# Kernel optimization log

Hardware: AMD Instinct MI355X
Metric: run time of the kernel (lower is better)

Reference implementation:

```python
import jax, jax.numpy as jnp
import numpy as np

B, L, D, H, DH, DI, NL, V = 1, 2048, 1024, 16, 64, 4096, 12, 32000
EPS = 1e-5  # torch LayerNorm default eps
SCALE = 1.0 / DH ** 0.5


def _ln(x):
    # LayerNorm with elementwise_affine=False
    m = jnp.mean(x, axis=-1, keepdims=True)
    va = jnp.var(x, axis=-1, keepdims=True)
    return (x - m) / jnp.sqrt(va + EPS)


def setup_inputs() -> dict:
    key = jax.random.key(0)
    ks = jax.random.split(key, 12)
    s = 0.02
    return {
        "X": jax.random.randint(ks[0], (B, L), 0, V),
        "Y": jax.random.randint(ks[1], (B, L), 0, V),
        "emb": jax.random.normal(ks[2], (V, D), jnp.float32) * s,
        "u": jax.random.normal(ks[3], (H, DH), jnp.float32) * s,
        "v": jax.random.normal(ks[4], (H, DH), jnp.float32) * s,
        "Wqkv": jax.random.normal(ks[5], (NL, 3 * H * DH, D), jnp.float32) * s,
        "Wpe": jax.random.normal(ks[6], (NL, H * DH, D), jnp.float32) * s,
        "Wout": jax.random.normal(ks[7], (NL, D, H * DH), jnp.float32) * s,
        "W1": jax.random.normal(ks[8], (NL, DI, D), jnp.float32) * s,
        "b1": jnp.zeros((NL, DI), jnp.float32),
        "W2": jax.random.normal(ks[9], (NL, D, DI), jnp.float32) * s,
        "b2": jnp.zeros((NL, D), jnp.float32),
        "Wc": jax.random.normal(ks[10], (V, D), jnp.float32) * s,
        "bc": jnp.zeros((V,), jnp.float32),
    }


def _forward(X, emb, u, v, Wqkv, Wpe, Wout, W1, b1, W2, b2, Wc, bc):
    q_len = X.shape[1]
    k_len = q_len  # mems=None -> m_len=0
    h = emb[X]  # (B, L, D); d_embedding == d_model so no projection

    # sinusoidal relative position embedding over descending positions
    pos = jnp.arange(k_len - 1, -1, -1, dtype=h.dtype)
    inv_freq = 1.0 / (10000.0 ** (jnp.arange(0, D, 2, dtype=h.dtype) / D))
    pp = pos[:, None] * inv_freq[None, :]              # (k, D/2)
    pe = jnp.concatenate([jnp.sin(pp), jnp.cos(pp)], axis=1)[None]  # (1, k, D)

    # causal mask: triu(ones, diagonal=1 + m_len), m_len=0; True = masked
    mask = jnp.triu(jnp.ones((q_len, k_len), bool), k=1)

    def layer(hid, params):
        wqkv, wpe, wout, w1, bb1, w2, bb2 = params
        qkv = hid @ wqkv.T                              # (B, q, 3HD)
        Q, K, Vv = jnp.split(qkv, 3, axis=-1)
        Q = Q.reshape(B, q_len, H, DH)
        K = K.reshape(B, k_len, H, DH)
        Vv = Vv.reshape(B, k_len, H, DH)
        r = (pe @ wpe.T).reshape(B, k_len, H, DH)       # requires B == 1
        AC = jnp.einsum('bqhd,bkhd->bhqk', Q + u, K)
        # NOTE: original code calls relative_shift(BD) but DISCARDS the result,
        # so BD is used unshifted — we reproduce that faithfully.
        BD = jnp.einsum('bqhd,bkhd->bhqk', Q + v, r)
        score = (AC + BD) * SCALE
        score = jnp.where(mask[None, None], -jnp.inf, score)
        prob = jax.nn.softmax(score, axis=-1)
        av = jnp.einsum('bhqk,bkhd->bqhd', prob, Vv).reshape(B, q_len, H * DH)
        hid = _ln(hid + av @ wout.T)                    # post-norm attention
        ff = jax.nn.relu(hid @ w1.T + bb1) @ w2.T + bb2
        hid = _ln(hid + ff)                             # post-norm FFN
        return hid, None

    h, _ = jax.lax.scan(layer, h, (Wqkv, Wpe, Wout, W1, b1, W2, b2))
    logits = h @ Wc.T + bc                              # (B, L, V)
    return logits.reshape(B * q_len, V)


def reference(X, Y, emb, u, v, Wqkv, Wpe, Wout, W1, b1, W2, b2, Wc, bc):
    # Y only determines y_len; here y_len == q_len so the full hidden is used.
    return _forward(X, emb, u, v, Wqkv, Wpe, Wout, W1, b1, W2, b2, Wc, bc)
```

## Files before the change

### kernel.cpp

```cpp
#include <hip/hip_runtime.h>
#include <hip/hip_bf16.h>

#define L_ 2048
#define D_ 1024
#define H_ 16
#define DH_ 64
#define DI_ 4096
#define NL_ 12
#define V_ 32000
#define EPS_ 1e-5f
#define SCALE_ 0.125f
#define LOG2E_ 1.44269504f
#define KBLK 64

typedef __attribute__((ext_vector_type(8))) short short8;
typedef __attribute__((ext_vector_type(4))) float f32x4;
typedef __hip_bfloat16 bf16;

__device__ __forceinline__ void gload_lds16(const void* g, void* l) {
  __builtin_amdgcn_global_load_lds((const __attribute__((address_space(1))) void*)g,
                                   (__attribute__((address_space(3))) void*)l, 16, 0, 0);
}

template<int STORE_BF16, int BIAS, int RELU, int SPLITK>
__global__ __launch_bounds__(256)
void gemm_bt(const bf16* __restrict__ A, const bf16* __restrict__ B,
             void* __restrict__ C, const float* __restrict__ bias,
             int M, int N, int K, int lda, int ldb, int ldc,
             long long Astride, long long Bstride, long long Cstride,
             float alpha, int Kc)
{
  __shared__ __align__(16) bf16 Atile[2][128 * 32];
  __shared__ __align__(16) bf16 Btile[2][128 * 32];

  const int gx = gridDim.x;
  const int nwg = gx * gridDim.y;
  const int orig = blockIdx.x + gx * blockIdx.y;
  const int qq = nwg >> 3, rr = nwg & 7;
  const int xcd = orig & 7, sidx = orig >> 3;
  const int lin = (xcd < rr ? xcd * (qq + 1) : rr * (qq + 1) + (xcd - rr) * qq) + sidx;
  const int m0 = (lin % gx) * 128;
  const int n0 = (lin / gx) * 128;

  const int z = blockIdx.z;
  int kbeg, kend;
  const bf16 *Ab, *Bb;
  size_t czoff;
  if (SPLITK) {
    kbeg = z * Kc; kend = kbeg + Kc;
    Ab = A; Bb = B;
    czoff = (size_t)z * (size_t)Cstride;
  } else {
    kbeg = 0; kend = K;
    Ab = A + (size_t)z * (size_t)Astride;
    Bb = B + (size_t)z * (size_t)Bstride;
    czoff = (size_t)z * (size_t)Cstride;
  }

  const int t = threadIdx.x;
  const int lane = t & 63;
  const int w = t >> 6;
  const int wm = w >> 1;
  const int wn = w & 1;
  const int rl = lane & 15;
  const int kl = (lane >> 4) << 3;

  const int r0 = t >> 2, kk0 = (t & 3) << 3;
  const int r1 = (256 + t) >> 2, kk1 = ((256 + t) & 3) << 3;
  int rb0 = n0 + r0; if (rb0 >= N) rb0 = N - 1;
  int rb1 = n0 + r1; if (rb1 >= N) rb1 = N - 1;

  f32x4 zero = {0.f, 0.f, 0.f, 0.f};
  f32x4 acc[4][4];
#pragma unroll
  for (int i = 0; i < 4; ++i)
#pragma unroll
    for (int j = 0; j < 4; ++j) acc[i][j] = zero;

  auto stage = [&](int buf, int k0) {
    gload_lds16(Ab + (size_t)(m0 + r0) * lda + (k0 + kk0), Atile[buf] + w * 512);
    gload_lds16(Bb + (size_t)rb0 * ldb + (k0 + kk0),       Btile[buf] + w * 512);
    gload_lds16(Ab + (size_t)(m0 + r1) * lda + (k0 + kk1), Atile[buf] + 2048 + w * 512);
    gload_lds16(Bb + (size_t)rb1 * ldb + (k0 + kk1),       Btile[buf] + 2048 + w * 512);
  };

  stage(0, kbeg);
  __syncthreads();

  int cur = 0;
  for (int k0 = kbeg; k0 < kend; k0 += 32) {
    if (k0 + 32 < kend) stage(cur ^ 1, k0 + 32);

    short8 af[4], bf_[4];
#pragma unroll
    for (int fm = 0; fm < 4; ++fm)
      af[fm] = *(const short8*)(Atile[cur] + (wm * 64 + fm * 16 + rl) * 32 + kl);
#pragma unroll
    for (int fn = 0; fn < 4; ++fn)
      bf_[fn] = *(const short8*)(Btile[cur] + (wn * 64 + fn * 16 + rl) * 32 + kl);
#pragma unroll
    for (int fm = 0; fm < 4; ++fm)
#pragma unroll
      for (int fn = 0; fn < 4; ++fn)
        acc[fm][fn] = __builtin_amdgcn_mfma_f32_16x16x32_bf16(af[fm], bf_[fn], acc[fm][fn], 0, 0, 0);
    __syncthreads();
    cur ^= 1;
  }

  const int row_l = (lane >> 4) << 2;
  const int col_l = lane & 15;
#pragma unroll
  for (int fm = 0; fm < 4; ++fm) {
#pragma unroll
    for (int fn = 0; fn < 4; ++fn) {
#pragma unroll
      for (int j = 0; j < 4; ++j) {
        const int m = m0 + wm * 64 + fm * 16 + row_l + j;
        const int n = n0 + wn * 64 + fn * 16 + col_l;
        if (m < M && n < N) {
          float vv = acc[fm][fn][j] * alpha;
          if (BIAS) vv += bias[n];
          if (RELU) vv = fmaxf(vv, 0.f);
          if (STORE_BF16)
            ((bf16*)C)[czoff + (size_t)m * ldc + n] = __float2bfloat16(vv);
          else
            ((float*)C)[czoff + (size_t)m * ldc + n] = vv;
        }
      }
    }
  }
}

__global__ __launch_bounds__(512)
void gemm256(const bf16* __restrict__ A, const bf16* __restrict__ B,
             float* __restrict__ C, const float* __restrict__ bias,
             int lda, int ldb, int ldc, int K)
{
  __shared__ __align__(16) bf16 As[2][256 * 64];
  __shared__ __align__(16) bf16 Bs[2][256 * 64];

  const int gx = gridDim.x;
  const int nwg = gx * gridDim.y;
  const int orig = blockIdx.x + gx * blockIdx.y;
  const int qq = nwg >> 3, rr = nwg & 7;
  const int xcd = orig & 7, sidx = orig >> 3;
  const int lin = (xcd < rr ? xcd * (qq + 1) : rr * (qq + 1) + (xcd - rr) * qq) + sidx;
  const int m0 = (lin % gx) * 256;
  const int n0 = (lin / gx) * 256;

  const int t = threadIdx.x;
  const int lane = t & 63, w = t >> 6;
  const int wm = w >> 2, wn = w & 3;
  const int rl = lane & 15, hi = lane >> 4;

  int srow[4], skb[4];
#pragma unroll
  for (int r = 0; r < 4; ++r) {
    int o = r * 8192 + t * 16;
    int s = o ^ (((o >> 9) & 1) << 5);
    srow[r] = s >> 7;
    skb[r] = s & 127;
  }

  auto stage = [&](int c, int kt) {
    const int k0 = kt * 64;
#pragma unroll
    for (int r = 0; r < 4; ++r)
      gload_lds16((const char*)A + ((size_t)(m0 + srow[r]) * lda + k0) * 2 + skb[r],
                  (char*)As[c] + r * 8192 + w * 1024);
#pragma unroll
    for (int r = 0; r < 4; ++r)
      gload_lds16((const char*)B + ((size_t)(n0 + srow[r]) * ldb + k0) * 2 + skb[r],
                  (char*)Bs[c] + r * 8192 + w * 1024);
  };

  f32x4 acc[8][4];
#pragma unroll
  for (int i = 0; i < 8; ++i)
#pragma unroll
    for (int j = 0; j < 4; ++j) acc[i][j] = (f32x4){0.f, 0.f, 0.f, 0.f};

  const int NT = K >> 6;
  stage(0, 0);
  stage(1, 1);
  asm volatile("s_waitcnt vmcnt(8)" ::: "memory");
  __builtin_amdgcn_s_barrier();
  asm volatile("" ::: "memory");

  int cur = 0;
  for (int kt = 0; kt < NT; ++kt) {
    short8 b[4][2];
#pragma unroll
    for (int nf = 0; nf < 4; ++nf)
#pragma unroll
      for (int ks = 0; ks < 2; ++ks) {
        int l = ((wn * 64 + nf * 16 + rl) << 7) + ks * 64 + hi * 16;
        b[nf][ks] = *(const short8*)((char*)Bs[cur] + (l ^ (((l >> 9) & 1) << 5)));
      }
#pragma unroll
    for (int p = 0; p < 4; ++p) {
      short8 a[2][2];
#pragma unroll
      for (int i = 0; i < 2; ++i)
#pragma unroll
        for (int ks = 0; ks < 2; ++ks) {
          int l = ((wm * 128 + (2 * p + i) * 16 + rl) << 7) + ks * 64 + hi * 16;
          a[i][ks] = *(const short8*)((char*)As[cur] + (l ^ (((l >> 9) & 1) << 5)));
        }
      __builtin_amdgcn_s_setprio(1);
#pragma unroll
      for (int i = 0; i < 2; ++i)
#pragma unroll
        for (int nf = 0; nf < 4; ++nf) {
          acc[2 * p + i][nf] = __builtin_amdgcn_mfma_f32_16x16x32_bf16(a[i][0], b[nf][0], acc[2 * p + i][nf], 0, 0, 0);
          acc[2 * p + i][nf] = __builtin_amdgcn_mfma_f32_16x16x32_bf16(a[i][1], b[nf][1], acc[2 * p + i][nf], 0, 0, 0);
        }
      __builtin_amdgcn_s_setprio(0);
      __builtin_amdgcn_sched_barrier(0);
    }
    __builtin_amdgcn_s_barrier();
    asm volatile("" ::: "memory");
    if (kt + 2 < NT) stage(cur, kt + 2);
    if (kt + 1 < NT) {
      if (kt + 2 < NT) asm volatile("s_waitcnt vmcnt(8)" ::: "memory");
      else             asm volatile("s_waitcnt vmcnt(0)" ::: "memory");
      __builtin_amdgcn_s_barrier();
      asm volatile("" ::: "memory");
    }
    cur ^= 1;
  }

#pragma unroll
  for (int mf = 0; mf < 8; ++mf) {
#pragma unroll
    for (int nf = 0; nf < 4; ++nf) {
#pragma unroll
      for (int j = 0; j < 4; ++j) {
        const int m = m0 + wm * 128 + mf * 16 + hi * 4 + j;
        const int n = n0 + wn * 64 + nf * 16 + rl;
        C[(size_t)m * ldc + n] = acc[mf][nf][j] + bias[n];
      }
    }
  }
}

__global__ __launch_bounds__(256)
void gemm_qkvpe(const bf16* __restrict__ Ah, const bf16* __restrict__ Ape,
                const bf16* __restrict__ Wqkv, const bf16* __restrict__ Wpe,
                const float* __restrict__ u, const float* __restrict__ v,
                bf16* __restrict__ QuQv, bf16* __restrict__ Kr, bf16* __restrict__ Vrm)
{
  __shared__ __align__(16) bf16 Atile[2][128 * 32];
  __shared__ __align__(16) bf16 Btile[2][128 * 32];

  const int gx = gridDim.x;
  const int nwg = gx * gridDim.y;
  const int orig = blockIdx.x + gx * blockIdx.y;
  const int qq = nwg >> 3, rr = nwg & 7;
  const int xcd = orig & 7, sidx = orig >> 3;
  const int lin = (xcd < rr ? xcd * (qq + 1) : rr * (qq + 1) + (xcd - rr) * qq) + sidx;
  const int m0 = (lin % gx) * 128;
  const int n0 = (lin / gx) * 128;

  const bf16* Ab = (n0 < 3072) ? Ah : Ape;
  const bf16* Bb = (n0 < 3072) ? (Wqkv + (size_t)n0 * D_) : (Wpe + (size_t)(n0 - 3072) * D_);

  const int t = threadIdx.x;
  const int lane = t & 63;
  const int w = t >> 6;
  const int wm = w >> 1;
  const int wn = w & 1;
  const int rl = lane & 15;
  const int kl = (lane >> 4) << 3;

  const int r0 = t >> 2, kk0 = (t & 3) << 3;
  const int r1 = (256 + t) >> 2, kk1 = ((256 + t) & 3) << 3;

  f32x4 zero = {0.f, 0.f, 0.f, 0.f};
  f32x4 acc[4][4];
#pragma unroll
  for (int i = 0; i < 4; ++i)
#pragma unroll
    for (int j = 0; j < 4; ++j) acc[i][j] = zero;

  auto stage = [&](int buf, int k0) {
    gload_lds16(Ab + (size_t)(m0 + r0) * D_ + (k0 + kk0), Atile[buf] + w * 512);
    gload_lds16(Bb + (size_t)r0 * D_ + (k0 + kk0),        Btile[buf] + w * 512);
    gload_lds16(Ab + (size_t)(m0 + r1) * D_ + (k0 + kk1), Atile[buf] + 2048 + w * 512);
    gload_lds16(Bb + (size_t)r1 * D_ + (k0 + kk1),        Btile[buf] + 2048 + w * 512);
  };

  stage(0, 0);
  __syncthreads();

  int cur = 0;
  for (int k0 = 0; k0 < D_; k0 += 32) {
    if (k0 + 32 < D_) stage(cur ^ 1, k0 + 32);

    short8 af[4], bf_[4];
#pragma unroll
    for (int fm = 0; fm < 4; ++fm)
      af[fm] = *(const short8*)(Atile[cur] + (wm * 64 + fm * 16 + rl) * 32 + kl);
#pragma unroll
    for (int fn = 0; fn < 4; ++fn)
      bf_[fn] = *(const short8*)(Btile[cur] + (wn * 64 + fn * 16 + rl) * 32 + kl);
#pragma unroll
    for (int fm = 0; fm < 4; ++fm)
#pragma unroll
      for (int fn = 0; fn < 4; ++fn)
        acc[fm][fn] = __builtin_amdgcn_mfma_f32_16x16x32_bf16(af[fm], bf_[fn], acc[fm][fn], 0, 0, 0);
    __syncthreads();
    cur ^= 1;
  }

  const int row_l = (lane >> 4) << 2;
  const int col_l = lane & 15;
#pragma unroll
  for (int fm = 0; fm < 4; ++fm) {
#pragma unroll
    for (int fn = 0; fn < 4; ++fn) {
#pragma unroll
      for (int j = 0; j < 4; ++j) {
        const int m = m0 + wm * 64 + fm * 16 + row_l + j;
        const int n = n0 + wn * 64 + fn * 16 + col_l;
        float x = acc[fm][fn][j];
        if (n < 1024) {
          const int h = n >> 6, d = n & 63;
          size_t b = ((size_t)h * L_ + m) * 128;
          QuQv[b + d]      = __float2bfloat16((x + u[n]) * SCALE_);
          QuQv[b + 64 + d] = __float2bfloat16((x + v[n]) * SCALE_);
        } else if (n < 2048) {
          const int n2 = n - 1024;
          Kr[(((size_t)(n2 >> 6)) * L_ + m) * 128 + (n2 & 63)] = __float2bfloat16(x);
        } else if (n < 3072) {
          Vrm[(size_t)m * 1024 + (n - 2048)] = __float2bfloat16(x);
        } else {
          const int c = n - 3072;
          Kr[(((size_t)(c >> 6)) * L_ + m) * 128 + 64 + (c & 63)] = __float2bfloat16(x);
        }
      }
    }
  }
}

__global__ __launch_bounds__(256)
void attn_fused(const bf16* __restrict__ QuQv, const bf16* __restrict__ Kr,
                const bf16* __restrict__ VT, bf16* __restrict__ av)
{
  __shared__ __align__(16) bf16 Kt[KBLK * 128];
  __shared__ __align__(16) bf16 Vt[DH_ * KBLK];
  __shared__ __align__(16) bf16 Pt[4][16 * KBLK];

  const int bid = blockIdx.x;
  const int tile = (bid < 256) ? (31 - (bid >> 4)) : ((bid - 256) >> 4);
  const int head = bid & 15;
  const int q0 = tile * 64;
  const int t = threadIdx.x, lane = t & 63, w = t >> 6;
  const int rl = lane & 15, hi = lane >> 4;

  const bf16* Qh = QuQv + (size_t)head * L_ * 128;
  const bf16* Kh = Kr   + (size_t)head * L_ * 128;
  const bf16* Vh = VT   + (size_t)head * DH_ * L_;

  const int qw0 = q0 + w * 16;

  short8 qf[4];
#pragma unroll
  for (int ks = 0; ks < 4; ++ks)
    qf[ks] = *(const short8*)(Qh + (size_t)(qw0 + rl) * 128 + ks * 32 + hi * 8);

  f32x4 o[4];
  float m_r[4], l_r[4];
#pragma unroll
  for (int j = 0; j < 4; ++j) { m_r[j] = -INFINITY; l_r[j] = 0.f; }
#pragma unroll
  for (int fn = 0; fn < 4; ++fn) o[fn] = (f32x4){0.f, 0.f, 0.f, 0.f};

  short8 kreg[4], vreg[2];
  auto load_regs = [&](int k0) {
#pragma unroll
    for (int i = 0; i < 4; ++i) {
      int c = i * 256 + t;
      int row = c >> 4, d8 = (c & 15) << 3;
      kreg[i] = *(const short8*)(Kh + (size_t)(k0 + row) * 128 + d8);
    }
#pragma unroll
    for (int i = 0; i < 2; ++i) {
      int c = i * 256 + t;
      int d = c >> 3, k8 = (c & 7) << 3;
      vreg[i] = *(const short8*)(Vh + (size_t)d * L_ + k0 + k8);
    }
  };
  auto write_lds = [&]() {
#pragma unroll
    for (int i = 0; i < 4; ++i) {
      int c = i * 256 + t;
      int row = c >> 4, d8 = (c & 15) << 3;
      int off = (row << 8) + (((d8 << 1)) ^ ((row & 7) << 4));
      *(short8*)((char*)Kt + off) = kreg[i];
    }
#pragma unroll
    for (int i = 0; i < 2; ++i) {
      int c = i * 256 + t;
      int d = c >> 3, k8 = (c & 7) << 3;
      int off = (d << 7) + (((k8 << 1)) ^ ((d & 7) << 4));
      *(short8*)((char*)Vt + off) = vreg[i];
    }
  };

  load_regs(0);
  write_lds();
  __syncthreads();

  const int kend = q0 + 64;
  for (int k0 = 0; k0 < kend; k0 += KBLK) {
    const bool more = (k0 + KBLK) < kend;
    if (more) load_regs(k0 + KBLK);

    if (k0 <= qw0 + 15) {
      f32x4 s[4];
#pragma unroll
      for (int fn = 0; fn < 4; ++fn) s[fn] = (f32x4){0.f, 0.f, 0.f, 0.f};
      __builtin_amdgcn_s_setprio(1);
#pragma unroll
      for (int fn = 0; fn < 4; ++fn) {
        const int krow = fn * 16 + rl;
#pragma unroll
        for (int ks = 0; ks < 4; ++ks) {
          short8 kf = *(const short8*)((char*)Kt + (krow << 8) +
                        ((((ks * 32 + hi * 8) << 1)) ^ ((krow & 7) << 4)));
          s[fn] = __builtin_amdgcn_mfma_f32_16x16x32_bf16(qf[ks], kf, s[fn], 0, 0, 0);
        }
      }
      __builtin_amdgcn_s_setprio(0);
      if (k0 + KBLK > q0) {
#pragma unroll
        for (int fn = 0; fn < 4; ++fn) {
          const int key = k0 + fn * 16 + rl;
#pragma unroll
          for (int j = 0; j < 4; ++j)
            if (key > qw0 + hi * 4 + j) s[fn][j] = -1e30f;
        }
      }
      float mx[4];
#pragma unroll
      for (int j = 0; j < 4; ++j)
        mx[j] = fmaxf(fmaxf(s[0][j], s[1][j]), fmaxf(s[2][j], s[3][j]));
#pragma unroll
      for (int off = 1; off < 16; off <<= 1)
#pragma unroll
        for (int j = 0; j < 4; ++j) mx[j] = fmaxf(mx[j], __shfl_xor(mx[j], off));
      float sf[4];
#pragma unroll
      for (int j = 0; j < 4; ++j) {
        float mn = fmaxf(m_r[j], mx[j]);
        sf[j] = exp2f((m_r[j] - mn) * LOG2E_);
        m_r[j] = mn;
      }
      float rs[4] = {0.f, 0.f, 0.f, 0.f};
#pragma unroll
      for (int fn = 0; fn < 4; ++fn) {
#pragma unroll
        for (int j = 0; j < 4; ++j) {
          float p = exp2f((s[fn][j] - m_r[j]) * LOG2E_);
          rs[j] += p;
          int row = hi * 4 + j;
          *(bf16*)((char*)Pt[w] + (row << 7) +
                   ((((fn * 16 + rl) << 1)) ^ ((row & 7) << 4))) = __float2bfloat16(p);
        }
      }
#pragma unroll
      for (int off = 1; off < 16; off <<= 1)
#pragma unroll
        for (int j = 0; j < 4; ++j) rs[j] += __shfl_xor(rs[j], off);
#pragma unroll
      for (int j = 0; j < 4; ++j) l_r[j] = l_r[j] * sf[j] + rs[j];
#pragma unroll
      for (int fn = 0; fn < 4; ++fn)
#pragma unroll
        for (int j = 0; j < 4; ++j) o[fn][j] *= sf[j];

      __builtin_amdgcn_s_setprio(1);
#pragma unroll
      for (int ks2 = 0; ks2 < 2; ++ks2) {
        short8 pa = *(const short8*)((char*)Pt[w] + (rl << 7) +
                      ((ks2 * 64 + hi * 16) ^ ((rl & 7) << 4)));
#pragma unroll
        for (int fn = 0; fn < 4; ++fn) {
          const int drow = fn * 16 + rl;
          short8 vf = *(const short8*)((char*)Vt + (drow << 7) +
                        ((ks2 * 64 + hi * 16) ^ ((drow & 7) << 4)));
          o[fn] = __builtin_amdgcn_mfma_f32_16x16x32_bf16(pa, vf, o[fn], 0, 0, 0);
        }
      }
      __builtin_amdgcn_s_setprio(0);
    }

    if (more) {
      __syncthreads();
      write_lds();
      __syncthreads();
    }
  }

#pragma unroll
  for (int fn = 0; fn < 4; ++fn) {
#pragma unroll
    for (int j = 0; j < 4; ++j) {
      int q = qw0 + hi * 4 + j;
      float vv = o[fn][j] / l_r[j];
      av[(size_t)q * D_ + head * 64 + fn * 16 + rl] = __float2bfloat16(vv);
    }
  }
}

__global__ __launch_bounds__(256)
void embed_k(const int* __restrict__ X, const float* __restrict__ emb,
             float* __restrict__ hout, bf16* __restrict__ hbout)
{
  int idx = blockIdx.x * 256 + threadIdx.x;
  if (idx >= L_ * D_) return;
  int tpos = idx >> 10, d = idx & 1023;
  float vv = emb[(size_t)X[tpos] * D_ + d];
  hout[idx] = vv;
  hbout[idx] = __float2bfloat16(vv);
}

__global__ __launch_bounds__(256)
void pe_k(bf16* __restrict__ pe)
{
  int idx = blockIdx.x * 256 + threadIdx.x;
  if (idx >= L_ * D_) return;
  int k = idx >> 10, i = idx & 1023;
  int f = (i < 512) ? i : (i - 512);
  float invf = exp2f(-(float)(2 * f) * (13.28771238f / 1024.f));
  float pp = (float)(L_ - 1 - k) * invf;
  float vv = (i < 512) ? sinf(pp) : cosf(pp);
  pe[idx] = __float2bfloat16(vv);
}

__global__ __launch_bounds__(256)
void cast_all(const float* __restrict__ wqkv, const float* __restrict__ wpe,
              const float* __restrict__ wout, const float* __restrict__ w1,
              const float* __restrict__ w2,
              bf16* __restrict__ dqkv, bf16* __restrict__ dpe, bf16* __restrict__ dout,
              bf16* __restrict__ d1, bf16* __restrict__ d2)
{
  const int n4 = 13631488 / 4;
  for (int i = blockIdx.x * 256 + threadIdx.x; i < n4; i += gridDim.x * 256) {
    int j = i * 4;
    const float* src; bf16* dst; int o;
    if (j < 3145728)      { src = wqkv; dst = dqkv; o = j; }
    else if (j < 4194304) { src = wpe;  dst = dpe;  o = j - 3145728; }
    else if (j < 5242880) { src = wout; dst = dout; o = j - 4194304; }
    else if (j < 9437184) { src = w1;   dst = d1;   o = j - 5242880; }
    else                  { src = w2;   dst = d2;   o = j - 9437184; }
    float4 vv = *(const float4*)(src + o);
    dst[o + 0] = __float2bfloat16(vv.x);
    dst[o + 1] = __float2bfloat16(vv.y);
    dst[o + 2] = __float2bfloat16(vv.z);
    dst[o + 3] = __float2bfloat16(vv.w);
  }
}

__global__ __launch_bounds__(256)
void cast_bf4(const float* __restrict__ in, bf16* __restrict__ out, long long n4)
{
  for (long long i = (long long)blockIdx.x * 256 + threadIdx.x; i < n4; i += (long long)gridDim.x * 256) {
    float4 vv = *(const float4*)(in + i * 4);
    out[i * 4 + 0] = __float2bfloat16(vv.x);
    out[i * 4 + 1] = __float2bfloat16(vv.y);
    out[i * 4 + 2] = __float2bfloat16(vv.z);
    out[i * 4 + 3] = __float2bfloat16(vv.w);
  }
}

__global__ __launch_bounds__(256)
void vtrans(const bf16* __restrict__ Vrm, bf16* __restrict__ VT)
{
  __shared__ unsigned short tile[64 * 65];
  const int q0 = blockIdx.x * 64;
  const int h = blockIdx.y;
  const int t = threadIdx.x;
#pragma unroll
  for (int i = 0; i < 2; ++i) {
    int qrow = i * 32 + (t >> 3);
    int d0 = (t & 7) * 8;
    short8 vv = *(const short8*)(Vrm + (size_t)(q0 + qrow) * 1024 + h * 64 + d0);
#pragma unroll
    for (int e = 0; e < 8; ++e)
      tile[(d0 + e) * 65 + qrow] = (unsigned short)vv[e];
  }
  __syncthreads();
  const int dr = t >> 5;
  const int q2 = (t & 31) * 2;
#pragma unroll
  for (int i = 0; i < 8; ++i) {
    int dd = i * 8 + dr;
    unsigned int pk = (unsigned int)tile[dd * 65 + q2] |
                      ((unsigned int)tile[dd * 65 + q2 + 1] << 16);
    *(unsigned int*)(VT + ((size_t)h * 64 + dd) * L_ + q0 + q2) = pk;
  }
}

__global__ __launch_bounds__(256)
void ln_residual(const float* __restrict__ resid, const float* __restrict__ parts,
                 int nparts, long long pstride, const float* __restrict__ bias,
                 float* __restrict__ hout, bf16* __restrict__ hbout)
{
  const int row = blockIdx.x;
  const int t = threadIdx.x;
  const int lane = t & 63, w = t >> 6;
  const size_t base = (size_t)row * D_;
  __shared__ float rs[4], rs2[4];
  float4 xv = *(const float4*)(resid + base + t * 4);
  for (int p = 0; p < nparts; ++p) {
    float4 pv = *(const float4*)(parts + (size_t)p * pstride + base + t * 4);
    xv.x += pv.x; xv.y += pv.y; xv.z += pv.z; xv.w += pv.w;
  }
  if (bias) {
    float4 bv = *(const float4*)(bias + t * 4);
    xv.x += bv.x; xv.y += bv.y; xv.z += bv.z; xv.w += bv.w;
  }
  float s = xv.x + xv.y + xv.z + xv.w;
  float s2 = xv.x * xv.x + xv.y * xv.y + xv.z * xv.z + xv.w * xv.w;
#pragma unroll
  for (int off = 32; off; off >>= 1) {
    s += __shfl_down(s, off);
    s2 += __shfl_down(s2, off);
  }
  if (lane == 0) { rs[w] = s; rs2[w] = s2; }
  __syncthreads();
  float S = rs[0] + rs[1] + rs[2] + rs[3];
  float S2 = rs2[0] + rs2[1] + rs2[2] + rs2[3];
  float mean = S * (1.f / D_);
  float var = S2 * (1.f / D_) - mean * mean;
  float inv = 1.f / sqrtf(var + EPS_);
  float4 y;
  y.x = (xv.x - mean) * inv;
  y.y = (xv.y - mean) * inv;
  y.z = (xv.z - mean) * inv;
  y.w = (xv.w - mean) * inv;
  *(float4*)(hout + base + t * 4) = y;
  __hip_bfloat162 p0, p1;
  p0.x = __float2bfloat16(y.x); p0.y = __float2bfloat16(y.y);
  p1.x = __float2bfloat16(y.z); p1.y = __float2bfloat16(y.w);
  *(__hip_bfloat162*)(hbout + base + t * 4)     = p0;
  *(__hip_bfloat162*)(hbout + base + t * 4 + 2) = p1;
}

extern "C" void kernel_launch(void* const* d_in, const int* in_sizes, int n_in,
                              void* d_out, int out_size, void* d_ws, size_t ws_size,
                              hipStream_t stream)
{
  (void)in_sizes; (void)n_in; (void)out_size; (void)ws_size;
  const int*   X    = (const int*)d_in[0];
  const float* emb  = (const float*)d_in[2];
  const float* u    = (const float*)d_in[3];
  const float* v    = (const float*)d_in[4];
  const float* Wqkv = (const float*)d_in[5];
  const float* Wpe  = (const float*)d_in[6];
  const float* Wout = (const float*)d_in[7];
  const float* W1   = (const float*)d_in[8];
  const float* b1   = (const float*)d_in[9];
  const float* W2   = (const float*)d_in[10];
  const float* b2   = (const float*)d_in[11];
  const float* Wc   = (const float*)d_in[12];
  const float* bc   = (const float*)d_in[13];
  float* out = (float*)d_out;

  size_t off = 0;
  auto alloc = [&](size_t bytes) {
    void* p = (char*)d_ws + off;
    off += (bytes + 255) & ~(size_t)255;
    return p;
  };
  float* h_f32   = (float*)alloc((size_t)L_ * D_ * 4);
  bf16*  h_bf    = (bf16*) alloc((size_t)L_ * D_ * 2);
  bf16*  pe_bf   = (bf16*) alloc((size_t)L_ * D_ * 2);
  bf16*  QuQv    = (bf16*) alloc((size_t)H_ * L_ * 128 * 2);
  bf16*  Kr      = (bf16*) alloc((size_t)H_ * L_ * 128 * 2);
  bf16*  Vrm     = (bf16*) alloc((size_t)L_ * D_ * 2);
  bf16*  VT      = (bf16*) alloc((size_t)H_ * DH_ * L_ * 2);
  bf16*  av_bf   = (bf16*) alloc((size_t)L_ * D_ * 2);
  float* part_f  = (float*)alloc((size_t)4 * L_ * D_ * 4);
  bf16*  ff1_bf  = (bf16*) alloc((size_t)L_ * DI_ * 2);
  bf16*  Wc_bf   = (bf16*) alloc((size_t)V_ * D_ * 2);
  bf16*  Wqkv_bf = (bf16*) alloc((size_t)3 * D_ * D_ * 2);
  bf16*  Wpe_bf  = (bf16*) alloc((size_t)D_ * D_ * 2);
  bf16*  Wout_bf = (bf16*) alloc((size_t)D_ * D_ * 2);
  bf16*  W1_bf   = (bf16*) alloc((size_t)DI_ * D_ * 2);
  bf16*  W2_bf   = (bf16*) alloc((size_t)D_ * DI_ * 2);

  const int eb = (L_ * D_ + 255) / 256;
  const long long LD = (long long)L_ * D_;

  embed_k<<<eb, 256, 0, stream>>>(X, emb, h_f32, h_bf);
  pe_k<<<eb, 256, 0, stream>>>(pe_bf);

  dim3 gqkvpe(L_ / 128, 4096 / 128, 1);
  dim3 gsk4(L_ / 128, D_ / 128, 4);
  dim3 gff1(L_ / 128, DI_ / 128, 1);

  for (int l = 0; l < NL_; ++l) {
    cast_all<<<2048, 256, 0, stream>>>(
        Wqkv + (size_t)l * 3 * D_ * D_, Wpe + (size_t)l * D_ * D_,
        Wout + (size_t)l * D_ * D_, W1 + (size_t)l * DI_ * D_, W2 + (size_t)l * D_ * DI_,
        Wqkv_bf, Wpe_bf, Wout_bf, W1_bf, W2_bf);

    gemm_qkvpe<<<gqkvpe, 256, 0, stream>>>(h_bf, pe_bf, Wqkv_bf, Wpe_bf, u, v, QuQv, Kr, Vrm);

    vtrans<<<dim3(L_ / 64, H_, 1), 256, 0, stream>>>(Vrm, VT);

    attn_fused<<<512, 256, 0, stream>>>(QuQv, Kr, VT, av_bf);

    gemm_bt<0, 0, 0, 1><<<gsk4, 256, 0, stream>>>(av_bf, Wout_bf, part_f, nullptr,
        L_, D_, D_, D_, D_, D_, 0, 0, LD, 1.f, 256);
    ln_residual<<<L_, 256, 0, stream>>>(h_f32, part_f, 4, LD, nullptr, h_f32, h_bf);

    gemm_bt<1, 1, 1, 0><<<gff1, 256, 0, stream>>>(h_bf, W1_bf, ff1_bf, b1 + (size_t)l * DI_,
        L_, DI_, D_, D_, D_, DI_, 0, 0, 0, 1.f, 0);

    gemm_bt<0, 0, 0, 1><<<gsk4, 256, 0, stream>>>(ff1_bf, W2_bf, part_f, nullptr,
        L_, D_, DI_, DI_, DI_, D_, 0, 0, LD, 1.f, 1024);
    ln_residual<<<L_, 256, 0, stream>>>(h_f32, part_f, 4, LD, b2 + (size_t)l * D_, h_f32, h_bf);
  }

  cast_bf4<<<2048, 256, 0, stream>>>(Wc, Wc_bf, (long long)V_ * D_ / 4);
  dim3 gl(L_ / 256, V_ / 256, 1);
  gemm256<<<gl, 512, 0, stream>>>(h_bf, Wc_bf, out, bc, D_, D_, V_, D_);
}
```

Measured before the change: 2.935 ms.

## Deepen GEMM prefetch to two tiles in flight with partial vmcnt waits

Both bf16 MFMA GEMM main loops now issue loads two K-tiles ahead and wait with s_waitcnt vmcnt(4) so the newest tile's loads can stay outstanding. The previous loop ended with a __syncthreads, which drains all memory counters. Each iteration now uses two raw barriers: one to free the buffer and one after the partial wait. s_setprio(1) is also wrapped around the MFMA block to favour the math wavefronts. The aim is to hide global-to-LDS latency better. The cost is an extra barrier per iteration and reliance on hand-tuned waitcnt correctness.

```diff
diff --git a/kernel.cpp b/kernel.cpp
--- a/kernel.cpp
+++ b/kernel.cpp
@@ -84,13 +84,19 @@
     gload_lds16(Bb + (size_t)rb1 * ldb + (k0 + kk1),       Btile[buf] + 2048 + w * 512);
   };
 
+  const int NT = (kend - kbeg) >> 5;
   stage(0, kbeg);
-  __syncthreads();
-
-  int cur = 0;
-  for (int k0 = kbeg; k0 < kend; k0 += 32) {
-    if (k0 + 32 < kend) stage(cur ^ 1, k0 + 32);
-
+  if (NT > 1) {
+    stage(1, kbeg + 32);
+    asm volatile("s_waitcnt vmcnt(4)" ::: "memory");
+  } else {
+    asm volatile("s_waitcnt vmcnt(0)" ::: "memory");
+  }
+  __builtin_amdgcn_s_barrier();
+  asm volatile("" ::: "memory");
+
+  for (int it = 0; it < NT; ++it) {
+    const int cur = it & 1;
     short8 af[4], bf_[4];
 #pragma unroll
     for (int fm = 0; fm < 4; ++fm)
@@ -98,13 +104,22 @@
 #pragma unroll
     for (int fn = 0; fn < 4; ++fn)
       bf_[fn] = *(const short8*)(Btile[cur] + (wn * 64 + fn * 16 + rl) * 32 + kl);
+    __builtin_amdgcn_s_setprio(1);
 #pragma unroll
     for (int fm = 0; fm < 4; ++fm)
 #pragma unroll
       for (int fn = 0; fn < 4; ++fn)
         acc[fm][fn] = __builtin_amdgcn_mfma_f32_16x16x32_bf16(af[fm], bf_[fn], acc[fm][fn], 0, 0, 0);
-    __syncthreads();
-    cur ^= 1;
+    __builtin_amdgcn_s_setprio(0);
+    __builtin_amdgcn_s_barrier();
+    asm volatile("" ::: "memory");
+    if (it + 2 < NT) stage(cur, kbeg + (it + 2) * 32);
+    if (it + 1 < NT) {
+      if (it + 2 < NT) asm volatile("s_waitcnt vmcnt(4)" ::: "memory");
+      else             asm volatile("s_waitcnt vmcnt(0)" ::: "memory");
+      __builtin_amdgcn_s_barrier();
+      asm volatile("" ::: "memory");
+    }
   }
 
   const int row_l = (lane >> 4) << 2;
@@ -290,13 +305,15 @@
     gload_lds16(Bb + (size_t)r1 * D_ + (k0 + kk1),        Btile[buf] + 2048 + w * 512);
   };
 
+  const int NT = D_ >> 5;
   stage(0, 0);
-  __syncthreads();
-
-  int cur = 0;
-  for (int k0 = 0; k0 < D_; k0 += 32) {
-    if (k0 + 32 < D_) stage(cur ^ 1, k0 + 32);
-
+  stage(1, 32);
+  asm volatile("s_waitcnt vmcnt(4)" ::: "memory");
+  __builtin_amdgcn_s_barrier();
+  asm volatile("" ::: "memory");
+
+  for (int it = 0; it < NT; ++it) {
+    const int cur = it & 1;
     short8 af[4], bf_[4];
 #pragma unroll
     for (int fm = 0; fm < 4; ++fm)
@@ -304,13 +321,22 @@
 #pragma unroll
     for (int fn = 0; fn < 4; ++fn)
       bf_[fn] = *(const short8*)(Btile[cur] + (wn * 64 + fn * 16 + rl) * 32 + kl);
+    __builtin_amdgcn_s_setprio(1);
 #pragma unroll
     for (int fm = 0; fm < 4; ++fm)
 #pragma unroll
       for (int fn = 0; fn < 4; ++fn)
         acc[fm][fn] = __builtin_amdgcn_mfma_f32_16x16x32_bf16(af[fm], bf_[fn], acc[fm][fn], 0, 0, 0);
-    __syncthreads();
-    cur ^= 1;
+    __builtin_amdgcn_s_setprio(0);
+    __builtin_amdgcn_s_barrier();
+    asm volatile("" ::: "memory");
+    if (it + 2 < NT) stage(cur, (it + 2) * 32);
+    if (it + 1 < NT) {
+      if (it + 2 < NT) asm volatile("s_waitcnt vmcnt(4)" ::: "memory");
+      else             asm volatile("s_waitcnt vmcnt(0)" ::: "memory");
+      __builtin_amdgcn_s_barrier();
+      asm volatile("" ::: "memory");
+    }
   }
 
   const int row_l = (lane >> 4) << 2;
```

Result: slower. 3.030 ms (+3.2%).
